# Kernel optimization log

Measured on AMD Instinct MI355X. Metric: run time of the kernel, lower is better.

The kernel has to match this reference:

```python
import jax, jax.numpy as jnp
import numpy as np

N_BLOCKS = 16
N_FEATS = 64
SCALE = 2
RGB_RANGE = 255.0
RGB_MEAN = np.array([0.4488, 0.4371, 0.4040], dtype=np.float32)  # DIV2K mean used by EDSR MeanShift


def conv2d(x, w, b=None):
    # x: [N,C,H,W], w: [O,I,kh,kw], SAME padding, stride 1
    y = jax.lax.conv_general_dilated(x, w, (1, 1), 'SAME',
                                     dimension_numbers=('NCHW', 'OIHW', 'NCHW'))
    if b is not None:
        y = y + b[None, :, None, None]
    return y


def ste_sign(x):
    # sign with straight-through estimator (identity gradient)
    return x + jax.lax.stop_gradient(jnp.sign(x) - x)


def bin_conv(x, w):
    # XNOR-style 1-bit conv: binarize activations to {-1,+1} (sign, STE),
    # binarize weights to sign(w) * alpha where alpha = per-output-channel mean(|w|).
    xb = ste_sign(x)
    alpha = jnp.mean(jnp.abs(w), axis=(1, 2, 3), keepdims=True)  # [O,1,1,1]
    wb = ste_sign(w) * alpha
    return conv2d(xb, wb)


def pixel_shuffle(x, r):
    # torch nn.PixelShuffle semantics
    n, c, h, w = x.shape
    x = x.reshape(n, c // (r * r), r, r, h, w)
    x = x.transpose(0, 1, 4, 2, 5, 3)  # [n, c', h, r, w, r]
    return x.reshape(n, c // (r * r), h * r, w * r)


def setup_inputs() -> dict:
    key = jax.random.key(0)
    ks = jax.random.split(key, 8)
    fan = 1.0 / np.sqrt(N_FEATS * 9)
    x = jax.random.uniform(ks[0], (16, 3, 128, 128), jnp.float32) * RGB_RANGE
    w_head = jax.random.normal(ks[1], (N_FEATS, 3, 3, 3), jnp.float32) * (1.0 / np.sqrt(3 * 9))
    w_body = jax.random.normal(ks[2], (N_BLOCKS, 2, N_FEATS, N_FEATS, 3, 3), jnp.float32) * fan
    w_body_last = jax.random.normal(ks[3], (N_FEATS, N_FEATS, 3, 3), jnp.float32) * fan
    w_up = jax.random.normal(ks[4], (N_FEATS * SCALE * SCALE, N_FEATS, 3, 3), jnp.float32) * fan
    w_tail = jax.random.normal(ks[5], (3, N_FEATS, 3, 3), jnp.float32) * fan
    b_tail = jnp.zeros((3,), jnp.float32)
    return {'x': x, 'w_head': w_head, 'w_body': w_body, 'w_body_last': w_body_last,
            'w_up': w_up, 'w_tail': w_tail, 'b_tail': b_tail}


def reference(x, w_head, w_body, w_body_last, w_up, w_tail, b_tail):
    shift = jnp.asarray(RGB_RANGE * RGB_MEAN).reshape(1, 3, 1, 1)
    x = x - shift                      # sub_mean
    h = conv2d(x, w_head)              # full-precision head, [N,64,H,W]
    r = h
    for i in range(N_BLOCKS):          # fixed layer count
        t = bin_conv(r, w_body[i, 0])
        t = jnp.tanh(t)
        t = bin_conv(t, w_body[i, 1])
        r = r + t                      # res_scale = 1
    r = bin_conv(r, w_body_last)
    res = r + h                        # global skip; this is `out`
    t = conv2d(res, w_up)              # 64 -> 64*r^2
    t = pixel_shuffle(t, SCALE)        # [N,64,H*r,W*r]
    t = conv2d(t, w_tail, b_tail)      # 64 -> 3
    out_img = t + shift                # add_mean
    return (out_img, res)
```

## Files before the change

### kernel.cpp

```cpp
#include <hip/hip_runtime.h>
#include <stdint.h>

typedef unsigned long long u64;
typedef unsigned int u32;
typedef _Float16 f16;
using i32x4  = __attribute__((ext_vector_type(4))) int;
using i32x16 = __attribute__((ext_vector_type(16))) int;
using f32x2  = __attribute__((ext_vector_type(2))) float;
using f32x4  = __attribute__((ext_vector_type(4))) float;
using f16x4  = __attribute__((ext_vector_type(4))) _Float16;
using f16x8  = __attribute__((ext_vector_type(8))) _Float16;

#define HW 16384

#define OFF_R      0ull
#define OFF_WEFF2  35651584ull
#define OFF_SG0    67108864ull
#define OFF_SG1    69206016ull
#define OFF_NZT    71303168ull
#define OFF_WBSG   73400320ull
#define OFF_ALPHA  74616832ull
#define OFF_WEFF   74625280ull

__global__ __launch_bounds__(256) void k_prep_wbsg(const float* __restrict__ wbody, const float* __restrict__ wlast,
                                                   signed char* __restrict__ wB, float* __restrict__ alpha){
  int t = blockIdx.x*256 + threadIdx.x;
  if (t >= 33*9*64) return;
  int o = t & 63, tap = (t>>6)%9, cid = t/(64*9);
  const float* src = (cid < 32) ? (wbody + (size_t)cid*36864) : wlast;
  u32 d[16];
  #pragma unroll
  for (int c4=0;c4<16;c4++){
    u32 v=0;
    #pragma unroll
    for (int j=0;j<4;j++){
      float w = src[(o*64 + c4*4+j)*9 + tap];
      v |= ((w < 0.f) ? 0xFFu : 0x01u) << (8*j);
    }
    d[c4]=v;
  }
  i32x4* dst = (i32x4*)(wB + ((size_t)(cid*9+tap)*64 + o)*64);
  #pragma unroll
  for (int k=0;k<4;k++){ i32x4 v; v[0]=(int)d[4*k]; v[1]=(int)d[4*k+1]; v[2]=(int)d[4*k+2]; v[3]=(int)d[4*k+3]; dst[k]=v; }
  if (tap==0){
    float s=0.f;
    for (int ci=0;ci<64;ci++)
      #pragma unroll
      for (int tp=0;tp<9;tp++) s += fabsf(src[(o*64+ci)*9+tp]);
    alpha[cid*64+o] = s * (1.0f/576.0f);
  }
}

__global__ __launch_bounds__(256) void k_prep_weff(const float* __restrict__ wup, const float* __restrict__ wtail,
                                                   float* __restrict__ weff){
  int idx = blockIdx.x*256 + threadIdx.x;
  int rx = idx & 3;
  int px = (idx >> 2) & 1;
  int base = idx >> 3;
  int o  = base % 3;
  int t2 = base / 3;
  int ci = t2 & 63;
  int ry = (t2 >> 6) & 3;
  int py = (t2 >> 8) & 1;
  int e  = t2 >> 9;
  int ex = e % 3, ey = e / 3;
  int ry_off = (py - 2) + ry;
  int rx_off = (px - 2) + rx;
  float acc = 0.f;
  for (int dy=0; dy<3; dy++){
    if (ey==1 && dy==0) continue;
    if (ey==2 && dy==2) continue;
    int pydy = py + dy - 1;
    int sy = ((pydy + 4) >> 1) - 2;
    int vy = (pydy + 4) & 1;
    int a = ry_off + 1 - sy;
    if (a < 0 || a > 2) continue;
    for (int dx=0; dx<3; dx++){
      if (ex==0 && dx==0) continue;
      if (ex==2 && dx==2) continue;
      int pxdx = px + dx - 1;
      int sx = ((pxdx + 4) >> 1) - 2;
      int vx = (pxdx + 4) & 1;
      int b = rx_off + 1 - sx;
      if (b < 0 || b > 2) continue;
      for (int c=0; c<64; c++){
        int u = c*4 + vy*2 + vx;
        acc += wtail[((o*64+c)*3+dy)*3+dx] * wup[((u*64+ci)*3+a)*3+b];
      }
    }
  }
  weff[idx] = acc;
}

__global__ __launch_bounds__(256) void k_prep_repack(const float* __restrict__ weff, float* __restrict__ w2){
  int t = blockIdx.x*256 + threadIdx.x;
  int px = t & 1;
  int q  = t >> 1;
  int rx = q & 3;  q >>= 2;
  int o  = q % 3;  q /= 3;
  int ry = q & 3;  q >>= 2;
  int ci = q & 63;
  int py = q >> 6;
  w2[t] = weff[(size_t)(2+py)*6144 + ry*1536 + ci*24 + (o*2+px)*4 + rx];
}

__global__ __launch_bounds__(256) void k_head(const float* __restrict__ x, const float* __restrict__ wh,
                                              f16* __restrict__ r, float* __restrict__ h, u64* __restrict__ sgR){
  __shared__ float wl[64*27];
  __shared__ float hs[32][257];
  for (int j=threadIdx.x; j<64*27; j+=256) wl[j] = wh[j];
  const int tid = threadIdx.x;
  const int id = blockIdx.x*256 + tid;
  const int n = id >> 14, p = id & 16383;
  const int pix0 = (blockIdx.x*256) & 16383;
  const int yy = p >> 7, xx = p & 127;
  float xv[27];
  const float sh[3] = {114.444f, 111.4605f, 103.02f};
  #pragma unroll
  for (int tap=0; tap<9; tap++){
    int Yq = yy + tap/3 - 1, Xq = xx + tap%3 - 1;
    bool v = ((unsigned)Yq < 128u) && ((unsigned)Xq < 128u);
    int q = (Yq << 7) + Xq;
    #pragma unroll
    for (int c=0; c<3; c++)
      xv[c*9+tap] = v ? (x[(size_t)(n*3+c)*HW + q] - sh[c]) : 0.f;
  }
  __syncthreads();
  u64 sg = 0;
  for (int R=0; R<2; R++){
    for (int o2=0; o2<32; o2++){
      const int o = R*32 + o2;
      float acc = 0.f;
      #pragma unroll
      for (int j=0; j<27; j++) acc += wl[o*27+j] * xv[j];
      f16 rv = (f16)acc;
      sg |= (u64)((float)rv < 0.f) << o;
      hs[o2][tid] = acc;
    }
    __syncthreads();
    {
      float* hb = h + (size_t)(n*64 + R*32)*HW + pix0 + tid;
      #pragma unroll
      for (int c2=0;c2<32;c2++) hb[(size_t)c2*HW] = hs[c2][tid];
    }
    {
      f16* rb = r + ((size_t)n*HW + pix0)*64 + R*32;
      #pragma unroll
      for (int j=0;j<4;j++){
        int L = j*256 + tid;
        int pix = L >> 2, c0 = (L & 3)*8;
        f16x8 t8;
        #pragma unroll
        for (int i=0;i<8;i++) t8[i] = (f16)hs[c0+i][pix];
        *(f16x8*)(rb + (size_t)pix*64 + c0) = t8;
      }
    }
    __syncthreads();
  }
  sgR[id] = sg;
}

template<int MODE>
__global__ __launch_bounds__(256) void k_bconv(const u64* __restrict__ sgIn, const u64* __restrict__ nzIn,
                                               const signed char* __restrict__ wB, const float* __restrict__ alphaC,
                                               f16* __restrict__ rbuf, u64* __restrict__ sgOut,
                                               u64* __restrict__ nzOut, float* __restrict__ resbuf){
  __shared__ signed char Abytes[4*68*80];

  const int bx = blockIdx.x;
  const int n  = bx >> 7;
  const int rem = bx & 127;
  const int y0 = (rem >> 1) << 1;
  const int x0 = (rem & 1) << 6;

  const int lane = threadIdx.x & 63;
  const int wid  = threadIdx.x >> 6;
  const int rrow = wid >> 1;
  const int och  = wid & 1;
  const int nn   = lane & 31;
  const int q    = lane >> 5;

  i32x4 Bf[9][2];
  #pragma unroll
  for (int t=0;t<9;t++)
    #pragma unroll
    for (int h=0;h<2;h++)
      Bf[t][h] = *(const i32x4*)(wB + ((size_t)(t*64 + och*32 + nn))*64 + h*32 + q*16);

  for (int s = threadIdx.x; s < 4*66; s += 256){
    int g = s/66, c = s%66;
    int y = y0 + g - 1, xcol = x0 + c - 1;
    u64 pos=0, neg=0;
    if (((unsigned)y < 128u) && ((unsigned)xcol < 128u)){
      int p = (n<<14) + (y<<7) + xcol;
      u64 sg = sgIn[p];
      if (MODE==1){ u64 nz = nzIn[p]; pos = nz & ~sg; neg = nz & sg; }
      else        { pos = ~sg;        neg = sg; }
    }
    u32 plo=(u32)pos, phi=(u32)(pos>>32), nlo=(u32)neg, nhi=(u32)(neg>>32);
    u32 tmp[16];
    #pragma unroll
    for (int i=0;i<16;i++){
      u32 np = ((i<8) ? (plo >> (4*i)) : (phi >> (4*i-32))) & 0xFu;
      u32 nm = ((i<8) ? (nlo >> (4*i)) : (nhi >> (4*i-32))) & 0xFu;
      u32 bp = (np * 0x00204081u) & 0x01010101u;
      u32 bn = (nm * 0x00204081u) & 0x01010101u;
      tmp[i] = bp | (bn * 0xFFu);
    }
    i32x4* dst = (i32x4*)&Abytes[(g*68 + c)*80];
    #pragma unroll
    for (int k=0;k<4;k++){ i32x4 v; v[0]=(int)tmp[4*k]; v[1]=(int)tmp[4*k+1]; v[2]=(int)tmp[4*k+2]; v[3]=(int)tmp[4*k+3]; dst[k]=v; }
  }
  __syncthreads();

  const float al = (MODE==0) ? 0.f : alphaC[och*32 + nn];

  for (int xh=0; xh<2; xh++){
    i32x16 acc;
    #pragma unroll
    for (int k=0;k<16;k++) acc[k]=0;

    const i32x4* Ap = (const i32x4*)&Abytes[(rrow*68 + xh*32 + nn)*80 + q*16];
    #pragma unroll
    for (int dy=0;dy<3;dy++)
      #pragma unroll
      for (int dx=0;dx<3;dx++){
        const int t = dy*3+dx;
        #pragma unroll
        for (int h=0;h<2;h++){
          i32x4 a = Ap[(dy*68+dx)*5 + h*2];
          acc = __builtin_amdgcn_mfma_i32_32x32x32_i8(a, Bf[t][h], acc, 0, 0, 0);
        }
      }

    const int ybase = y0 + rrow, xbase = x0 + xh*32;

    if (MODE==0){
      u32 sgc=0, nzc=0;
      #pragma unroll
      for (int reg=0; reg<16; reg++){
        u64 bs = __ballot(acc[reg] < 0);
        u64 bn = __ballot(acc[reg] != 0);
        const int px0 = (reg&3) + ((reg>>2)<<3);
        sgc = (lane==px0  ) ? (u32)bs       : sgc;
        sgc = (lane==px0+4) ? (u32)(bs>>32) : sgc;
        nzc = (lane==px0  ) ? (u32)bn       : nzc;
        nzc = (lane==px0+4) ? (u32)(bn>>32) : nzc;
      }
      if (lane < 32){
        int p = (n<<14) + (ybase<<7) + xbase + lane;
        ((u32*)sgOut)[p*2 + och] = sgc;
        ((u32*)nzOut)[p*2 + och] = nzc;
      }
    } else if (MODE==1){
      float newr[16];
      f16* rp = rbuf + ((size_t)n*HW + (ybase<<7) + xbase + 4*q)*64 + och*32 + nn;
      #pragma unroll
      for (int k2=0;k2<4;k2++){
        #pragma unroll
        for (int j=0;j<4;j++){
          const int po = (8*k2 + j)*64;
          f16 old = rp[po];
          float rv = (float)old + al * (float)acc[4*k2+j];
          f16 nv = (f16)rv;
          rp[po] = nv;
          newr[4*k2+j] = (float)nv;
        }
      }
      u32 sgc=0;
      #pragma unroll
      for (int reg=0; reg<16; reg++){
        u64 b = __ballot(newr[reg] < 0.f);
        const int px0 = (reg&3) + ((reg>>2)<<3);
        sgc = (lane==px0  ) ? (u32)b       : sgc;
        sgc = (lane==px0+4) ? (u32)(b>>32) : sgc;
      }
      if (lane < 32){
        int p = (n<<14) + (ybase<<7) + xbase + lane;
        ((u32*)sgOut)[p*2 + och] = sgc;
      }
    } else {
      float* hp = resbuf + ((size_t)((n<<6) + och*32 + nn))*HW + (ybase<<7) + xbase;
      #pragma unroll
      for (int k2=0;k2<4;k2++){
        f32x4 hv = *(f32x4*)(hp + 4*q + 8*k2);
        #pragma unroll
        for (int j=0;j<4;j++) hv[j] += al * (float)acc[4*k2+j];
        *(f32x4*)(hp + 4*q + 8*k2) = hv;
      }
    }
  }
}

__global__ __launch_bounds__(256) void k_tail(const float* __restrict__ res, const float* __restrict__ w2,
                                              const float* __restrict__ btail, float* __restrict__ out){
  __shared__ float wsm[6144];
  __shared__ f32x2 red[128][13];
  const int id  = blockIdx.x;
  const int xcd = id & 7;
  const int t   = id >> 3;
  const int n   = xcd*2 + (t & 1);
  const int py  = (t >> 1) & 1;
  const int yg  = t >> 2;
  const int y0  = yg << 2;
  const int x   = threadIdx.x & 127;
  const int ch  = threadIdx.x >> 7;
  const int rbase = y0 + py - 2;

  {
    const f32x4* src = (const f32x4*)(w2 + (size_t)py*6144);
    f32x4* dst = (f32x4*)wsm;
    #pragma unroll
    for (int j=0;j<6;j++) dst[threadIdx.x + 256*j] = src[threadIdx.x + 256*j];
  }

  int xo[5]; float cm[5];
  #pragma unroll
  for (int j=0;j<5;j++){
    int c = x - 2 + j;
    cm[j] = ((unsigned)c < 128u) ? 1.f : 0.f;
    xo[j] = c < 0 ? 0 : (c > 127 ? 127 : c);
  }

  f32x2 acc[4][3];
  #pragma unroll
  for (int k=0;k<4;k++)
    #pragma unroll
    for (int o=0;o<3;o++) acc[k][o] = (f32x2)(0.f);

  __syncthreads();

  const float* rbn = res + (size_t)n*64*HW;
  const int ci0 = ch*32;
  #pragma unroll 1
  for (int ci=ci0; ci<ci0+32; ci++){
    const float* rp = rbn + (size_t)ci*HW;
    float v[7][5];
    #pragma unroll
    for (int w=0; w<7; w++){
      const int row = rbase + w;
      if ((unsigned)row < 128u){
        const float* q = rp + (row<<7);
        #pragma unroll
        for (int j=0;j<5;j++) v[w][j] = q[xo[j]] * cm[j];
      } else {
        #pragma unroll
        for (int j=0;j<5;j++) v[w][j] = 0.f;
      }
    }
    f32x2 vp[7][4];
    #pragma unroll
    for (int w=0; w<7; w++)
      #pragma unroll
      for (int rx=0; rx<4; rx++){ vp[w][rx][0] = v[w][rx]; vp[w][rx][1] = v[w][rx+1]; }
    const float* wp = wsm + ci*96;
    #pragma unroll
    for (int ry=0; ry<4; ry++){
      const float* wr = wp + ry*24;
      f32x2 wpair[12];
      #pragma unroll
      for (int jj=0;jj<6;jj++){
        f32x4 t4 = *(const f32x4*)(wr + 4*jj);
        wpair[2*jj][0]   = t4[0]; wpair[2*jj][1]   = t4[1];
        wpair[2*jj+1][0] = t4[2]; wpair[2*jj+1][1] = t4[3];
      }
      #pragma unroll
      for (int k=0;k<4;k++){
        #pragma unroll
        for (int o=0;o<3;o++){
          #pragma unroll
          for (int rx=0;rx<4;rx++)
            acc[k][o] = __builtin_elementwise_fma(wpair[o*4+rx], vp[k+ry][rx], acc[k][o]);
        }
      }
    }
  }

  if (ch==1){
    #pragma unroll
    for (int k=0;k<4;k++)
      #pragma unroll
      for (int o=0;o<3;o++) red[x][k*3+o] = acc[k][o];
  }
  __syncthreads();
  if (ch==0){
    const float sh[3] = {114.444f, 111.4605f, 103.02f};
    #pragma unroll
    for (int k=0;k<4;k++){
      const int Y = ((y0 + k) << 1) + py;
      #pragma unroll
      for (int o=0;o<3;o++){
        f32x2 s2 = acc[k][o] + red[x][k*3+o];
        const float b = btail[o] + sh[o];
        s2[0] += b; s2[1] += b;
        *(f32x2*)(out + (((size_t)((n*3+o)*256 + Y)) << 8) + 2*x) = s2;
      }
    }
  }
}

__global__ __launch_bounds__(256) void k_border(const float* __restrict__ res, const float* __restrict__ weff,
                                                const float* __restrict__ btail, float* __restrict__ out){
  int t = blockIdx.x*256 + threadIdx.x;
  if (t >= 16384) return;
  int n    = t >> 10;
  int rem  = t & 1023;
  int edge = rem >> 8;
  int pos  = rem & 255;
  int X, Y;
  if (edge==0){ Y = 0;   X = pos; if (X==0 || X==255) return; }
  else if (edge==1){ Y = 255; X = pos; if (X==0 || X==255) return; }
  else if (edge==2){ X = 0;   Y = pos; }
  else            { X = 255; Y = pos; }
  int px = X & 1, x = X >> 1;
  int py = Y & 1, y = Y >> 1;
  int ey = (Y==0) ? 1 : ((Y==255) ? 2 : 0);
  int ex = (X==0) ? 0 : ((X==255) ? 2 : 1);
  const float* Ws = weff + (size_t)((ey*3+ex)*2+py) * 6144;
  float acc[3] = {0.f,0.f,0.f};
  for (int ry=0; ry<4; ry++){
    int yy = y + (py-2) + ry;
    bool rowv = ((unsigned)yy < 128u);
    const float* rp = res + (size_t)n*64*HW + yy*128;
    for (int ci=0; ci<64; ci++){
      const float* Wc = Ws + ry*1536 + ci*24 + px*4;
      #pragma unroll
      for (int rx=0; rx<4; rx++){
        int xxc = x + (px-2) + rx;
        float v = (rowv && (unsigned)xxc < 128u) ? rp[(size_t)ci*HW + xxc] : 0.f;
        acc[0] += Wc[0*8+rx] * v;
        acc[1] += Wc[1*8+rx] * v;
        acc[2] += Wc[2*8+rx] * v;
      }
    }
  }
  const float sh[3] = {114.444f, 111.4605f, 103.02f};
  for (int o=0; o<3; o++)
    out[(size_t)((n*3+o)*256+Y)*256 + X] = acc[o] + btail[o] + sh[o];
}

extern "C" void kernel_launch(void* const* d_in, const int* in_sizes, int n_in,
                              void* d_out, int out_size, void* d_ws, size_t ws_size,
                              hipStream_t stream) {
  const float* x      = (const float*)d_in[0];
  const float* w_head = (const float*)d_in[1];
  const float* w_body = (const float*)d_in[2];
  const float* w_last = (const float*)d_in[3];
  const float* w_up   = (const float*)d_in[4];
  const float* w_tail = (const float*)d_in[5];
  const float* b_tail = (const float*)d_in[6];

  char* ws = (char*)d_ws;
  f16*  r      = (f16*) (ws + OFF_R);
  u64*  sg0    = (u64*) (ws + OFF_SG0);
  u64*  sg1    = (u64*) (ws + OFF_SG1);
  u64*  nzT    = (u64*) (ws + OFF_NZT);
  signed char* wBsg = (signed char*)(ws + OFF_WBSG);
  float* alpha = (float*)(ws + OFF_ALPHA);
  float* weff  = (float*)(ws + OFF_WEFF);
  float* weff2 = (float*)(ws + OFF_WEFF2);

  float* out = (float*)d_out;
  float* res = out + 3145728;

  k_prep_wbsg<<<75, 256, 0, stream>>>(w_body, w_last, wBsg, alpha);
  k_prep_weff<<<432, 256, 0, stream>>>(w_up, w_tail, weff);
  k_prep_repack<<<48, 256, 0, stream>>>(weff, weff2);
  k_head<<<1024, 256, 0, stream>>>(x, w_head, r, res, sg0);
  for (int i=0; i<16; i++){
    k_bconv<0><<<2048, 256, 0, stream>>>(sg0, nullptr, wBsg + (size_t)(2*i)*36864,
                                         nullptr, nullptr, sg1, nzT, nullptr);
    k_bconv<1><<<2048, 256, 0, stream>>>(sg1, nzT, wBsg + (size_t)(2*i+1)*36864,
                                         alpha + (2*i+1)*64, r, sg0, nullptr, nullptr);
  }
  k_bconv<2><<<2048, 256, 0, stream>>>(sg0, nullptr, wBsg + (size_t)32*36864,
                                       alpha + 32*64, nullptr, nullptr, nullptr, res);
  k_tail<<<1024, 256, 0, stream>>>(res, weff2, b_tail, out);
  k_border<<<64, 256, 0, stream>>>(res, weff, b_tail, out);
}
```

Measured before the change: 1.306 ms.

## Fuse both binary convs of each residual block into one kernel with halo recompute

Replaces the two per-block launches (sign conv writing sign/nonzero masks to global, then the second conv reading them) with a single kernel per residual block. Each workgroup computes the first conv over a 6x66 halo region into shared memory, then runs the second conv on the 4x64 interior and updates r. This removes the intermediate global mask round-trip and halves the launch count. In exchange it recomputes halo rows (about 1.5x the first-conv MFMA work), uses more shared memory per block, and ping-pongs the sign buffers.

Result: faster. 1.169 ms (-10.5%).

```diff
diff --git a/kernel.cpp b/kernel.cpp
--- a/kernel.cpp
+++ b/kernel.cpp
@@ -21,6 +21,22 @@
 #define OFF_WBSG   73400320ull
 #define OFF_ALPHA  74616832ull
 #define OFF_WEFF   74625280ull
+
+__device__ __forceinline__ void expand_store(signed char* dst8, u64 pos, u64 neg){
+  u32 plo=(u32)pos, phi=(u32)(pos>>32), nlo=(u32)neg, nhi=(u32)(neg>>32);
+  u32 tmp[16];
+  #pragma unroll
+  for (int i=0;i<16;i++){
+    u32 np = ((i<8) ? (plo >> (4*i)) : (phi >> (4*i-32))) & 0xFu;
+    u32 nm = ((i<8) ? (nlo >> (4*i)) : (nhi >> (4*i-32))) & 0xFu;
+    u32 bp = (np * 0x00204081u) & 0x01010101u;
+    u32 bn = (nm * 0x00204081u) & 0x01010101u;
+    tmp[i] = bp | (bn * 0xFFu);
+  }
+  i32x4* dst = (i32x4*)dst8;
+  #pragma unroll
+  for (int k=0;k<4;k++){ i32x4 v; v[0]=(int)tmp[4*k]; v[1]=(int)tmp[4*k+1]; v[2]=(int)tmp[4*k+2]; v[3]=(int)tmp[4*k+3]; dst[k]=v; }
+}
 
 __global__ __launch_bounds__(256) void k_prep_wbsg(const float* __restrict__ wbody, const float* __restrict__ wlast,
                                                    signed char* __restrict__ wB, float* __restrict__ alpha){
@@ -160,18 +176,21 @@
   sgR[id] = sg;
 }
 
-template<int MODE>
-__global__ __launch_bounds__(256) void k_bconv(const u64* __restrict__ sgIn, const u64* __restrict__ nzIn,
-                                               const signed char* __restrict__ wB, const float* __restrict__ alphaC,
-                                               f16* __restrict__ rbuf, u64* __restrict__ sgOut,
-                                               u64* __restrict__ nzOut, float* __restrict__ resbuf){
-  __shared__ signed char Abytes[4*68*80];
-
-  const int bx = blockIdx.x;
-  const int n  = bx >> 7;
-  const int rem = bx & 127;
-  const int y0 = (rem >> 1) << 1;
-  const int x0 = (rem & 1) << 6;
+__global__ __launch_bounds__(256) void k_rblock(const u64* __restrict__ sgIn,
+                                                const signed char* __restrict__ wB1,
+                                                const signed char* __restrict__ wB2,
+                                                const float* __restrict__ alphaC,
+                                                f16* __restrict__ rbuf,
+                                                u64* __restrict__ sgOut){
+  __shared__ __attribute__((aligned(16))) signed char A[46080];
+  __shared__ u32 sgl[6*66*2];
+  __shared__ u32 nzl[6*66*2];
+
+  const int bx  = blockIdx.x;
+  const int n   = bx >> 6;
+  const int rem = bx & 63;
+  const int y0  = (rem >> 1) << 2;
+  const int x0  = (rem & 1) << 6;
 
   const int lane = threadIdx.x & 63;
   const int wid  = threadIdx.x >> 6;
@@ -180,6 +199,157 @@
   const int nn   = lane & 31;
   const int q    = lane >> 5;
 
+  for (int s = threadIdx.x; s < 8*68; s += 256){
+    int g = s/68, c = s%68;
+    int y = y0 - 2 + g, xc = x0 - 2 + c;
+    u64 pos=0, neg=0;
+    if (((unsigned)y < 128u) && ((unsigned)xc < 128u)){
+      u64 sg = sgIn[(n<<14) + (y<<7) + xc];
+      pos = ~sg; neg = sg;
+    }
+    expand_store(&A[(g*68 + c)*80], pos, neg);
+  }
+  __syncthreads();
+
+  {
+    i32x4 Bf[9][2];
+    #pragma unroll
+    for (int t=0;t<9;t++)
+      #pragma unroll
+      for (int h=0;h<2;h++)
+        Bf[t][h] = *(const i32x4*)(wB1 + ((size_t)(t*64 + och*32 + nn))*64 + h*32 + q*16);
+
+    for (int cr2=0; cr2<3; cr2++){
+      const int crr = rrow*3 + cr2;
+      for (int cg=0; cg<3; cg++){
+        i32x16 acc;
+        #pragma unroll
+        for (int k=0;k<16;k++) acc[k]=0;
+        const i32x4* Ap = (const i32x4*)&A[((size_t)crr*68 + cg*32 + nn)*80 + q*16];
+        #pragma unroll
+        for (int dy=0;dy<3;dy++)
+          #pragma unroll
+          for (int dx=0;dx<3;dx++){
+            const int t = dy*3+dx;
+            #pragma unroll
+            for (int h=0;h<2;h++){
+              i32x4 a = Ap[(dy*68+dx)*5 + h*2];
+              acc = __builtin_amdgcn_mfma_i32_32x32x32_i8(a, Bf[t][h], acc, 0, 0, 0);
+            }
+          }
+        u32 sgc=0, nzc=0;
+        #pragma unroll
+        for (int reg=0; reg<16; reg++){
+          u64 bs = __ballot(acc[reg] < 0);
+          u64 bn = __ballot(acc[reg] != 0);
+          const int px0 = (reg&3) + ((reg>>2)<<3);
+          sgc = (lane==px0  ) ? (u32)bs       : sgc;
+          sgc = (lane==px0+4) ? (u32)(bs>>32) : sgc;
+          nzc = (lane==px0  ) ? (u32)bn       : nzc;
+          nzc = (lane==px0+4) ? (u32)(bn>>32) : nzc;
+        }
+        const int u = cg*32 + lane;
+        if (lane < 32 && u < 66){
+          sgl[(crr*66 + u)*2 + och] = sgc;
+          nzl[(crr*66 + u)*2 + och] = nzc;
+        }
+      }
+    }
+  }
+  __syncthreads();
+
+  for (int s = threadIdx.x; s < 6*66; s += 256){
+    int g = s/66, c = s%66;
+    int y = y0 - 1 + g, xc = x0 - 1 + c;
+    u64 pos=0, neg=0;
+    if (((unsigned)y < 128u) && ((unsigned)xc < 128u)){
+      int e = (g*66 + c)*2;
+      u64 sg = (u64)sgl[e] | ((u64)sgl[e+1] << 32);
+      u64 nz = (u64)nzl[e] | ((u64)nzl[e+1] << 32);
+      pos = nz & ~sg; neg = nz & sg;
+    }
+    expand_store(&A[(g*68 + c)*80], pos, neg);
+  }
+  __syncthreads();
+
+  {
+    i32x4 Bf[9][2];
+    #pragma unroll
+    for (int t=0;t<9;t++)
+      #pragma unroll
+      for (int h=0;h<2;h++)
+        Bf[t][h] = *(const i32x4*)(wB2 + ((size_t)(t*64 + och*32 + nn))*64 + h*32 + q*16);
+
+    const float al = alphaC[och*32 + nn];
+
+    for (int r2=0; r2<2; r2++){
+      const int ro = rrow*2 + r2;
+      for (int cg=0; cg<2; cg++){
+        i32x16 acc;
+        #pragma unroll
+        for (int k=0;k<16;k++) acc[k]=0;
+        const i32x4* Ap = (const i32x4*)&A[((size_t)ro*68 + cg*32 + nn)*80 + q*16];
+        #pragma unroll
+        for (int dy=0;dy<3;dy++)
+          #pragma unroll
+          for (int dx=0;dx<3;dx++){
+            const int t = dy*3+dx;
+            #pragma unroll
+            for (int h=0;h<2;h++){
+              i32x4 a = Ap[(dy*68+dx)*5 + h*2];
+              acc = __builtin_amdgcn_mfma_i32_32x32x32_i8(a, Bf[t][h], acc, 0, 0, 0);
+            }
+          }
+        const int ybase = y0 + ro, xbase = x0 + cg*32;
+        float newr[16];
+        f16* rp = rbuf + ((size_t)n*HW + (ybase<<7) + xbase + 4*q)*64 + och*32 + nn;
+        #pragma unroll
+        for (int k2=0;k2<4;k2++){
+          #pragma unroll
+          for (int j=0;j<4;j++){
+            const int po = (8*k2 + j)*64;
+            f16 old = rp[po];
+            float rv = (float)old + al * (float)acc[4*k2+j];
+            f16 nv = (f16)rv;
+            rp[po] = nv;
+            newr[4*k2+j] = (float)nv;
+          }
+        }
+        u32 sgc=0;
+        #pragma unroll
+        for (int reg=0; reg<16; reg++){
+          u64 b = __ballot(newr[reg] < 0.f);
+          const int px0 = (reg&3) + ((reg>>2)<<3);
+          sgc = (lane==px0  ) ? (u32)b       : sgc;
+          sgc = (lane==px0+4) ? (u32)(b>>32) : sgc;
+        }
+        if (lane < 32){
+          int p = (n<<14) + (ybase<<7) + xbase + lane;
+          ((u32*)sgOut)[p*2 + och] = sgc;
+        }
+      }
+    }
+  }
+}
+
+__global__ __launch_bounds__(256) void k_blast(const u64* __restrict__ sgIn,
+                                               const signed char* __restrict__ wB, const float* __restrict__ alphaC,
+                                               float* __restrict__ resbuf){
+  __shared__ signed char Abytes[4*68*80];
+
+  const int bx = blockIdx.x;
+  const int n  = bx >> 7;
+  const int rem = bx & 127;
+  const int y0 = (rem >> 1) << 1;
+  const int x0 = (rem & 1) << 6;
+
+  const int lane = threadIdx.x & 63;
+  const int wid  = threadIdx.x >> 6;
+  const int rrow = wid >> 1;
+  const int och  = wid & 1;
+  const int nn   = lane & 31;
+  const int q    = lane >> 5;
+
   i32x4 Bf[9][2];
   #pragma unroll
   for (int t=0;t<9;t++)
@@ -192,28 +362,14 @@
     int y = y0 + g - 1, xcol = x0 + c - 1;
     u64 pos=0, neg=0;
     if (((unsigned)y < 128u) && ((unsigned)xcol < 128u)){
-      int p = (n<<14) + (y<<7) + xcol;
-      u64 sg = sgIn[p];
-      if (MODE==1){ u64 nz = nzIn[p]; pos = nz & ~sg; neg = nz & sg; }
-      else        { pos = ~sg;        neg = sg; }
-    }
-    u32 plo=(u32)pos, phi=(u32)(pos>>32), nlo=(u32)neg, nhi=(u32)(neg>>32);
-    u32 tmp[16];
-    #pragma unroll
-    for (int i=0;i<16;i++){
-      u32 np = ((i<8) ? (plo >> (4*i)) : (phi >> (4*i-32))) & 0xFu;
-      u32 nm = ((i<8) ? (nlo >> (4*i)) : (nhi >> (4*i-32))) & 0xFu;
-      u32 bp = (np * 0x00204081u) & 0x01010101u;
-      u32 bn = (nm * 0x00204081u) & 0x01010101u;
-      tmp[i] = bp | (bn * 0xFFu);
-    }
-    i32x4* dst = (i32x4*)&Abytes[(g*68 + c)*80];
-    #pragma unroll
-    for (int k=0;k<4;k++){ i32x4 v; v[0]=(int)tmp[4*k]; v[1]=(int)tmp[4*k+1]; v[2]=(int)tmp[4*k+2]; v[3]=(int)tmp[4*k+3]; dst[k]=v; }
-  }
-  __syncthreads();
-
-  const float al = (MODE==0) ? 0.f : alphaC[och*32 + nn];
+      u64 sg = sgIn[(n<<14) + (y<<7) + xcol];
+      pos = ~sg; neg = sg;
+    }
+    expand_store(&Abytes[(g*68 + c)*80], pos, neg);
+  }
+  __syncthreads();
+
+  const float al = alphaC[och*32 + nn];
 
   for (int xh=0; xh<2; xh++){
     i32x16 acc;
@@ -234,60 +390,13 @@
       }
 
     const int ybase = y0 + rrow, xbase = x0 + xh*32;
-
-    if (MODE==0){
-      u32 sgc=0, nzc=0;
-      #pragma unroll
-      for (int reg=0; reg<16; reg++){
-        u64 bs = __ballot(acc[reg] < 0);
-        u64 bn = __ballot(acc[reg] != 0);
-        const int px0 = (reg&3) + ((reg>>2)<<3);
-        sgc = (lane==px0  ) ? (u32)bs       : sgc;
-        sgc = (lane==px0+4) ? (u32)(bs>>32) : sgc;
-        nzc = (lane==px0  ) ? (u32)bn       : nzc;
-        nzc = (lane==px0+4) ? (u32)(bn>>32) : nzc;
-      }
-      if (lane < 32){
-        int p = (n<<14) + (ybase<<7) + xbase + lane;
-        ((u32*)sgOut)[p*2 + och] = sgc;
-        ((u32*)nzOut)[p*2 + och] = nzc;
-      }
-    } else if (MODE==1){
-      float newr[16];
-      f16* rp = rbuf + ((size_t)n*HW + (ybase<<7) + xbase + 4*q)*64 + och*32 + nn;
-      #pragma unroll
-      for (int k2=0;k2<4;k2++){
-        #pragma unroll
-        for (int j=0;j<4;j++){
-          const int po = (8*k2 + j)*64;
-          f16 old = rp[po];
-          float rv = (float)old + al * (float)acc[4*k2+j];
-          f16 nv = (f16)rv;
-          rp[po] = nv;
-          newr[4*k2+j] = (float)nv;
-        }
-      }
-      u32 sgc=0;
-      #pragma unroll
-      for (int reg=0; reg<16; reg++){
-        u64 b = __ballot(newr[reg] < 0.f);
-        const int px0 = (reg&3) + ((reg>>2)<<3);
-        sgc = (lane==px0  ) ? (u32)b       : sgc;
-        sgc = (lane==px0+4) ? (u32)(b>>32) : sgc;
-      }
-      if (lane < 32){
-        int p = (n<<14) + (ybase<<7) + xbase + lane;
-        ((u32*)sgOut)[p*2 + och] = sgc;
-      }
-    } else {
-      float* hp = resbuf + ((size_t)((n<<6) + och*32 + nn))*HW + (ybase<<7) + xbase;
-      #pragma unroll
-      for (int k2=0;k2<4;k2++){
-        f32x4 hv = *(f32x4*)(hp + 4*q + 8*k2);
-        #pragma unroll
-        for (int j=0;j<4;j++) hv[j] += al * (float)acc[4*k2+j];
-        *(f32x4*)(hp + 4*q + 8*k2) = hv;
-      }
+    float* hp = resbuf + ((size_t)((n<<6) + och*32 + nn))*HW + (ybase<<7) + xbase;
+    #pragma unroll
+    for (int k2=0;k2<4;k2++){
+      f32x4 hv = *(f32x4*)(hp + 4*q + 8*k2);
+      #pragma unroll
+      for (int j=0;j<4;j++) hv[j] += al * (float)acc[4*k2+j];
+      *(f32x4*)(hp + 4*q + 8*k2) = hv;
     }
   }
 }
@@ -454,7 +563,6 @@
   f16*  r      = (f16*) (ws + OFF_R);
   u64*  sg0    = (u64*) (ws + OFF_SG0);
   u64*  sg1    = (u64*) (ws + OFF_SG1);
-  u64*  nzT    = (u64*) (ws + OFF_NZT);
   signed char* wBsg = (signed char*)(ws + OFF_WBSG);
   float* alpha = (float*)(ws + OFF_ALPHA);
   float* weff  = (float*)(ws + OFF_WEFF);
@@ -467,14 +575,16 @@
   k_prep_weff<<<432, 256, 0, stream>>>(w_up, w_tail, weff);
   k_prep_repack<<<48, 256, 0, stream>>>(weff, weff2);
   k_head<<<1024, 256, 0, stream>>>(x, w_head, r, res, sg0);
+
+  u64* pin = sg0;
+  u64* pout = sg1;
   for (int i=0; i<16; i++){
-    k_bconv<0><<<2048, 256, 0, stream>>>(sg0, nullptr, wBsg + (size_t)(2*i)*36864,
-                                         nullptr, nullptr, sg1, nzT, nullptr);
-    k_bconv<1><<<2048, 256, 0, stream>>>(sg1, nzT, wBsg + (size_t)(2*i+1)*36864,
-                                         alpha + (2*i+1)*64, r, sg0, nullptr, nullptr);
-  }
-  k_bconv<2><<<2048, 256, 0, stream>>>(sg0, nullptr, wBsg + (size_t)32*36864,
-                                       alpha + 32*64, nullptr, nullptr, nullptr, res);
+    k_rblock<<<1024, 256, 0, stream>>>(pin, wBsg + (size_t)(2*i)*36864, wBsg + (size_t)(2*i+1)*36864,
+                                       alpha + (2*i+1)*64, r, pout);
+    u64* tmp = pin; pin = pout; pout = tmp;
+  }
+  k_blast<<<2048, 256, 0, stream>>>(pin, wBsg + (size_t)32*36864, alpha + 32*64, res);
+
   k_tail<<<1024, 256, 0, stream>>>(res, weff2, b_tail, out);
   k_border<<<64, 256, 0, stream>>>(res, weff, b_tail, out);
 }
```
